# Optimization experiments

Measured on AMD Instinct MI355X. Metric: run time of the kernel, lower is better.

The kernel has to match this reference:

```python
import jax, jax.numpy as jnp
import numpy as np

B, S, N, D = 4, 8, 1024, 512
PROJ_DIM = 512
HEADS = 4
EPSILON = 0.01


def pose_encoding(p):
    # p: [B,S,N,d]; faithful to PoseEncoding.__call__
    n, d = p.shape[-2], p.shape[-1]
    sin_d = d // 2 if d % 2 == 0 else (d - 1) // 2 + 1
    cos_d = d // 2 if d % 2 == 0 else (d - 1) // 2
    idx = jnp.arange(n, dtype=p.dtype)[:, None]
    ks = jnp.arange(sin_d, dtype=p.dtype)[None, :]
    kc = jnp.arange(cos_d, dtype=p.dtype)[None, :]
    sin_ape = jnp.sin(idx / (1000.0 * (2.0 * ks / d) + 0.01))  # [N, sin_d]
    cos_ape = jnp.cos(idx / (1000.0 * (2.0 * kc / d) + 0.01))  # [N, cos_d]
    pe = jnp.zeros((n, d), dtype=p.dtype)
    pe = pe.at[:, 0::2].set(sin_ape).at[:, 1::2].set(cos_ape)
    return p + pe


def setup_inputs() -> dict:
    key = jax.random.key(0)
    ks = jax.random.split(key, 5)
    x = jax.random.normal(ks[0], (B, S, N, D), dtype=jnp.float32)
    Wqkv = jax.random.normal(ks[1], (HEADS, D, 3 * D), dtype=jnp.float32) * 0.02
    bqkv = jax.random.normal(ks[2], (HEADS, 3 * D), dtype=jnp.float32) * 0.02
    Wp = jax.random.normal(ks[3], (HEADS, D, PROJ_DIM), dtype=jnp.float32) * 0.02
    bp = jax.random.normal(ks[4], (HEADS, PROJ_DIM), dtype=jnp.float32) * 0.02
    return {"x": x, "Wqkv": Wqkv, "bqkv": bqkv, "Wp": Wp, "bp": bp}


def reference(x, Wqkv, bqkv, Wp, bp):
    b, s, n, d = x.shape
    heads = Wqkv.shape[0]
    pred_proj = None
    proj = None
    for h in range(heads):  # small fixed loop over structurally distinct heads
        qkv = jax.nn.selu(jnp.einsum('bsnd,de->bsne', x, Wqkv[h]) + bqkv[h])
        qkv = qkv.reshape(b, s, n, 3, d)
        q, k, v = qkv[..., 0, :], qkv[..., 1, :], qkv[..., 2, :]
        # non-standard ordering: scale QK^T, multiply by V, THEN softmax
        qkT = jnp.einsum('bsnd,bsmd->bsnm', q, k) / d  # [B,S,N,N]
        att = jax.nn.softmax(jnp.einsum('bsnm,bsmd->bsnd', qkT, v), axis=-1)
        proj = jax.nn.gelu(jnp.einsum('bsnd,dp->bsnp', att, Wp[h]) + bp[h],
                           approximate=False)
        if pred_proj is None:
            pred_proj = proj
        else:
            proj = proj + EPSILON * pred_proj  # pred_proj stays = head-0 proj (as in source)
    return pose_encoding(proj)
```

## Files before the change

kernel.cpp:

```cpp
#include <hip/hip_runtime.h>
#include <hip/hip_bf16.h>
#include <math.h>

typedef unsigned short u16;
typedef unsigned int   u32;
typedef __bf16  v8bf  __attribute__((ext_vector_type(8)));
typedef float   v4f   __attribute__((ext_vector_type(4)));

#define EPS_H 0.01f

typedef const __attribute__((address_space(1))) void* gas_t;
typedef __attribute__((address_space(3))) void* las_t;
#define GL2LDS(g,l) __builtin_amdgcn_global_load_lds((gas_t)(const void*)(g), (las_t)(void*)(l), 16, 0, 0)

#define VMW8()   asm volatile("s_waitcnt vmcnt(8)" ::: "memory")
#define VMW0()   asm volatile("s_waitcnt vmcnt(0)" ::: "memory")
#define BAR()    __builtin_amdgcn_s_barrier()
#define SCHED0() __builtin_amdgcn_sched_barrier(0)

__device__ __forceinline__ u16 f2bf(float f) {
    __bf16 h = (__bf16)f;
    return *reinterpret_cast<u16*>(&h);
}
__device__ __forceinline__ float bfs(u16 v) { return __uint_as_float(((u32)v) << 16); }
__device__ __forceinline__ float selu_f(float x) {
    const float sc = 1.0507009873554805f, al = 1.6732632423543772f;
    return x > 0.f ? sc * x : sc * al * (__expf(x) - 1.0f);
}
__device__ __forceinline__ float gelu_f(float x) {
    return 0.5f * x * (1.f + erff(x * 0.7071067811865476f));
}
__device__ __forceinline__ float pe_val(int n, int j) {
    float t = 1000.0f * ((float)(j & ~1) * (1.0f / 512.0f)) + 0.01f;
    float a = (float)n / t;
    return (j & 1) ? cosf(a) : sinf(a);
}

__device__ __forceinline__ v8bf lfrag(const u16* base, int row, int lane) {
    int g = (lane >> 4) ^ ((row >> 1) & 3);
    return *(const v8bf*)((const char*)base + row * 64 + g * 16);
}

__device__ __forceinline__ void stage2(const u16* g, size_t gstride, u16* lds, int wave, int lane) {
    const int l2 = lane >> 2;
    #pragma unroll
    for (int i = 0; i < 4; ++i) {
        const int ib  = wave * 4 + i;
        const int sub = ib >> 3;
        const int rl  = (ib & 7) * 16 + l2;
        const int gs  = (lane & 3) ^ ((rl >> 1) & 3);
        GL2LDS((const char*)(g + (size_t)rl * gstride + sub * 32) + gs * 16,
               (char*)lds + ib * 1024);
    }
}

#define COMPUTE_TILE(Abuf, Bbuf)                                                   \
    {                                                                              \
        const u16* A0 = &(Abuf)[0];    const u16* A1 = &(Abuf)[4096];              \
        const u16* B0 = &(Bbuf)[0];    const u16* B1 = &(Bbuf)[4096];              \
        v8bf b0[4], b1[4];                                                         \
        _Pragma("unroll")                                                          \
        for (int fc = 0; fc < 4; ++fc) {                                           \
            const int brow = wn * 64 + fc * 16 + (lane & 15);                      \
            b0[fc] = lfrag(B0, brow, lane);                                        \
            b1[fc] = lfrag(B1, brow, lane);                                        \
        }                                                                          \
        __builtin_amdgcn_s_setprio(1);                                             \
        _Pragma("unroll")                                                          \
        for (int fr = 0; fr < 4; ++fr) {                                           \
            const int arow = wm * 64 + fr * 16 + (lane & 15);                      \
            v8bf a0 = lfrag(A0, arow, lane);                                       \
            v8bf a1 = lfrag(A1, arow, lane);                                       \
            _Pragma("unroll")                                                      \
            for (int fc = 0; fc < 4; ++fc) {                                       \
                acc[fr][fc] = __builtin_amdgcn_mfma_f32_16x16x32_bf16(a0, b0[fc], acc[fr][fc], 0, 0, 0); \
                acc[fr][fc] = __builtin_amdgcn_mfma_f32_16x16x32_bf16(a1, b1[fc], acc[fr][fc], 0, 0, 0); \
            }                                                                      \
        }                                                                          \
        __builtin_amdgcn_s_setprio(0);                                             \
    }

__global__ __launch_bounds__(256)
void k_prep(const float* __restrict__ x, u16* __restrict__ xbf, float* __restrict__ pe,
            const float* __restrict__ Wqkv, u16* __restrict__ WqT,
            const float* __restrict__ Wp, u16* __restrict__ WpT)
{
    __shared__ float t[32][33];
    const int b = blockIdx.x, tid = threadIdx.x;
    if (b < 8192) {
        const size_t i = ((size_t)b * 256 + tid) * 8;
        float4 a = *(const float4*)&x[i];
        float4 c = *(const float4*)&x[i + 4];
        ushort4 o0, o1;
        o0.x = f2bf(a.x); o0.y = f2bf(a.y); o0.z = f2bf(a.z); o0.w = f2bf(a.w);
        o1.x = f2bf(c.x); o1.y = f2bf(c.y); o1.z = f2bf(c.z); o1.w = f2bf(c.w);
        *(ushort4*)&xbf[i] = o0;
        *(ushort4*)&xbf[i + 4] = o1;
        return;
    }
    if (b < 10240) {
        int idx = (b - 8192) * 256 + tid;
        pe[idx] = pe_val(idx >> 9, idx & 511);
        return;
    }
    const float* src; u16* dst; int rows, cols, bx, by;
    if (b < 11776) {
        int l = b - 10240, hh = l / 768, rem = l % 768;
        bx = rem % 48; by = rem / 48;
        src = Wqkv + (size_t)(hh ? 3 : 0) * 786432; dst = WqT + (size_t)hh * 786432;
        rows = 512; cols = 1536;
    } else {
        int l = b - 11776, hh = l / 256, rem = l % 256;
        bx = rem % 16; by = rem / 16;
        src = Wp + (size_t)(hh ? 3 : 0) * 262144; dst = WpT + (size_t)hh * 262144;
        rows = 512; cols = 512;
    }
    const int c0 = bx * 32, r0 = by * 32;
    #pragma unroll
    for (int i = 0; i < 4; ++i) {
        int idx = tid + i * 256;
        int rr = idx >> 5, cc = idx & 31;
        t[rr][cc] = src[(size_t)(r0 + rr) * cols + c0 + cc];
    }
    __syncthreads();
    #pragma unroll
    for (int i = 0; i < 4; ++i) {
        int idx = tid + i * 256;
        int rr = idx >> 5, cc = idx & 31;
        dst[(size_t)(c0 + rr) * rows + r0 + cc] = f2bf(t[cc][rr]);
    }
}

__global__ __launch_bounds__(256, 1)
void k1_qkv(const u16* __restrict__ xbf, const u16* __restrict__ WT,
            const float* __restrict__ bias, u16* __restrict__ q,
            u16* __restrict__ kT, u16* __restrict__ vT, const int swzstride)
{
    __shared__ u16 Als[2][8192];
    __shared__ u16 Bls[2][8192];
    const int tid = threadIdx.x, lane = tid & 63, wave = tid >> 6;
    const int orig = blockIdx.x + blockIdx.y * 12;
    const int swz  = (orig & 7) * swzstride + (orig >> 3);
    const int col0 = (swz % 12) * 128, row0 = (swz / 12) * 128;
    const int wm = wave >> 1, wn = wave & 1;
    const u16* Ab = xbf + (size_t)row0 * 512;
    const u16* Bb = WT + (size_t)col0 * 512;
    v4f acc[4][4] = {};

    stage2(Ab,      512, &Als[0][0], wave, lane);
    stage2(Bb,      512, &Bls[0][0], wave, lane);
    stage2(Ab + 64, 512, &Als[1][0], wave, lane);
    stage2(Bb + 64, 512, &Bls[1][0], wave, lane);
    for (int t = 0; t < 8; ++t) {
        const int c = t & 1;
        if (t < 7) VMW8(); else VMW0();
        BAR(); SCHED0();
        COMPUTE_TILE(Als[c], Bls[c]);
        BAR(); SCHED0();
        if (t + 2 < 8) {
            const int k0 = (t + 2) * 64;
            stage2(Ab + k0, 512, &Als[c][0], wave, lane);
            stage2(Bb + k0, 512, &Bls[c][0], wave, lane);
        }
    }

    const int region = col0 >> 9;
    #pragma unroll
    for (int fn = 0; fn < 4; ++fn) {
        const int c = col0 + wn * 64 + fn * 16 + (lane & 15);
        const float bc = bias[c];
        #pragma unroll
        for (int fm = 0; fm < 4; ++fm) {
            const int rb = row0 + wm * 64 + fm * 16 + ((lane >> 4) << 2);
            float v0 = selu_f(acc[fm][fn][0] + bc);
            float v1 = selu_f(acc[fm][fn][1] + bc);
            float v2 = selu_f(acc[fm][fn][2] + bc);
            float v3 = selu_f(acc[fm][fn][3] + bc);
            if (region == 0) {
                q[(size_t)(rb + 0) * 512 + c] = f2bf(v0);
                q[(size_t)(rb + 1) * 512 + c] = f2bf(v1);
                q[(size_t)(rb + 2) * 512 + c] = f2bf(v2);
                q[(size_t)(rb + 3) * 512 + c] = f2bf(v3);
            } else {
                ushort4 st; st.x = f2bf(v0); st.y = f2bf(v1); st.z = f2bf(v2); st.w = f2bf(v3);
                const int seq = rb >> 10, n = rb & 1023;
                u16* dst = (region == 1) ? kT : vT;
                const int cc = c - ((region == 1) ? 512 : 1024);
                *(ushort4*)&dst[(size_t)seq * 524288 + (size_t)cc * 1024 + n] = st;
            }
        }
    }
}

__global__ __launch_bounds__(256, 1)
void k2_ktv(const u16* __restrict__ kT, const u16* __restrict__ vT, u16* __restrict__ Mt)
{
    __shared__ u16 Als[2][8192];
    __shared__ u16 Bls[2][8192];
    const int tid = threadIdx.x, lane = tid & 63, wave = tid >> 6;
    const int d0 = blockIdx.x * 128, p0 = blockIdx.y * 128, seq = blockIdx.z;
    const u16* Ab = kT + (size_t)seq * 524288 + (size_t)d0 * 1024;
    const u16* Bb = vT + (size_t)seq * 524288 + (size_t)p0 * 1024;
    const int wm = wave >> 1, wn = wave & 1;
    v4f acc[4][4] = {};

    stage2(Ab,      1024, &Als[0][0], wave, lane);
    stage2(Bb,      1024, &Bls[0][0], wave, lane);
    stage2(Ab + 64, 1024, &Als[1][0], wave, lane);
    stage2(Bb + 64, 1024, &Bls[1][0], wave, lane);
    for (int t = 0; t < 16; ++t) {
        const int c = t & 1;
        if (t < 15) VMW8(); else VMW0();
        BAR(); SCHED0();
        COMPUTE_TILE(Als[c], Bls[c]);
        BAR(); SCHED0();
        if (t + 2 < 16) {
            const int m0 = (t + 2) * 64;
            stage2(Ab + m0, 1024, &Als[c][0], wave, lane);
            stage2(Bb + m0, 1024, &Bls[c][0], wave, lane);
        }
    }

    #pragma unroll
    for (int fn = 0; fn < 4; ++fn) {
        const int p = p0 + wn * 64 + fn * 16 + (lane & 15);
        #pragma unroll
        for (int fm = 0; fm < 4; ++fm) {
            const int d = d0 + wm * 64 + fm * 16 + ((lane >> 4) << 2);
            ushort4 st;
            st.x = f2bf(acc[fm][fn][0] * (1.f / 512.f));
            st.y = f2bf(acc[fm][fn][1] * (1.f / 512.f));
            st.z = f2bf(acc[fm][fn][2] * (1.f / 512.f));
            st.w = f2bf(acc[fm][fn][3] * (1.f / 512.f));
            *(ushort4*)&Mt[(size_t)seq * 262144 + (size_t)p * 512 + d] = st;
        }
    }
}

__global__ __launch_bounds__(256, 1)
void k3a_s(const u16* __restrict__ q, const u16* __restrict__ Mt, u16* __restrict__ S,
           const int swzstride)
{
    __shared__ u16 Als[2][8192];
    __shared__ u16 Bls[2][8192];
    const int tid = threadIdx.x, lane = tid & 63, wave = tid >> 6;
    const int orig = blockIdx.x + blockIdx.y * 4;
    const int swz  = (orig & 7) * swzstride + (orig >> 3);
    const int p0 = (swz % 4) * 128, row0 = (swz / 4) * 128;
    const int seq = row0 >> 10;
    const u16* Ab = q + (size_t)row0 * 512;
    const u16* Bb = Mt + (size_t)seq * 262144 + (size_t)p0 * 512;
    const int wm = wave >> 1, wn = wave & 1;
    v4f acc[4][4] = {};

    stage2(Ab,      512, &Als[0][0], wave, lane);
    stage2(Bb,      512, &Bls[0][0], wave, lane);
    stage2(Ab + 64, 512, &Als[1][0], wave, lane);
    stage2(Bb + 64, 512, &Bls[1][0], wave, lane);
    for (int t = 0; t < 8; ++t) {
        const int c = t & 1;
        if (t < 7) VMW8(); else VMW0();
        BAR(); SCHED0();
        COMPUTE_TILE(Als[c], Bls[c]);
        BAR(); SCHED0();
        if (t + 2 < 8) {
            const int k0 = (t + 2) * 64;
            stage2(Ab + k0, 512, &Als[c][0], wave, lane);
            stage2(Bb + k0, 512, &Bls[c][0], wave, lane);
        }
    }

    #pragma unroll
    for (int fn = 0; fn < 4; ++fn) {
        const int c = p0 + wn * 64 + fn * 16 + (lane & 15);
        #pragma unroll
        for (int fm = 0; fm < 4; ++fm) {
            const int rb = row0 + wm * 64 + fm * 16 + ((lane >> 4) << 2);
            S[(size_t)(rb + 0) * 512 + c] = f2bf(acc[fm][fn][0]);
            S[(size_t)(rb + 1) * 512 + c] = f2bf(acc[fm][fn][1]);
            S[(size_t)(rb + 2) * 512 + c] = f2bf(acc[fm][fn][2]);
            S[(size_t)(rb + 3) * 512 + c] = f2bf(acc[fm][fn][3]);
        }
    }
}

__global__ __launch_bounds__(512)
void k3b_sm(u16* __restrict__ S)
{
    const int row  = blockIdx.x * 8 + (threadIdx.x >> 6);
    const int lane = threadIdx.x & 63;
    u16* rp = S + (size_t)row * 512 + lane * 8;
    ushort4 u0 = *(const ushort4*)rp;
    ushort4 u1 = *(const ushort4*)(rp + 4);
    float f[8] = {bfs(u0.x), bfs(u0.y), bfs(u0.z), bfs(u0.w),
                  bfs(u1.x), bfs(u1.y), bfs(u1.z), bfs(u1.w)};
    float m = f[0];
    #pragma unroll
    for (int j = 1; j < 8; ++j) m = fmaxf(m, f[j]);
    #pragma unroll
    for (int off = 32; off > 0; off >>= 1) m = fmaxf(m, __shfl_xor(m, off));
    float s = 0.f;
    #pragma unroll
    for (int j = 0; j < 8; ++j) { f[j] = __expf(f[j] - m); s += f[j]; }
    #pragma unroll
    for (int off = 32; off > 0; off >>= 1) s += __shfl_xor(s, off);
    const float inv = 1.0f / s;
    ushort4 o0, o1;
    o0.x = f2bf(f[0] * inv); o0.y = f2bf(f[1] * inv);
    o0.z = f2bf(f[2] * inv); o0.w = f2bf(f[3] * inv);
    o1.x = f2bf(f[4] * inv); o1.y = f2bf(f[5] * inv);
    o1.z = f2bf(f[6] * inv); o1.w = f2bf(f[7] * inv);
    *(ushort4*)rp = o0;
    *(ushort4*)(rp + 4) = o1;
}

__global__ __launch_bounds__(256, 1)
void k3c_proj(const u16* __restrict__ att, const u16* __restrict__ WpT,
              const float* __restrict__ bp, const float* __restrict__ pe,
              float* __restrict__ out, const int mode, const int rowbase, const int swzstride)
{
    __shared__ u16 Als[2][8192];
    __shared__ u16 Bls[2][8192];
    const int tid = threadIdx.x, lane = tid & 63, wave = tid >> 6;
    const int orig = blockIdx.x + blockIdx.y * 4;
    const int swz  = (orig & 7) * swzstride + (orig >> 3);
    const int e0 = (swz % 4) * 128, row0 = (swz / 4) * 128;
    const u16* Ab = att + (size_t)row0 * 512;
    const u16* Bb = WpT + (size_t)e0 * 512;
    const int wm = wave >> 1, wn = wave & 1;
    v4f acc[4][4] = {};

    stage2(Ab,      512, &Als[0][0], wave, lane);
    stage2(Bb,      512, &Bls[0][0], wave, lane);
    stage2(Ab + 64, 512, &Als[1][0], wave, lane);
    stage2(Bb + 64, 512, &Bls[1][0], wave, lane);
    for (int t = 0; t < 8; ++t) {
        const int c = t & 1;
        if (t < 7) VMW8(); else VMW0();
        BAR(); SCHED0();
        COMPUTE_TILE(Als[c], Bls[c]);
        BAR(); SCHED0();
        if (t + 2 < 8) {
            const int k0 = (t + 2) * 64;
            stage2(Ab + k0, 512, &Als[c][0], wave, lane);
            stage2(Bb + k0, 512, &Bls[c][0], wave, lane);
        }
    }

    #pragma unroll
    for (int fn = 0; fn < 4; ++fn) {
        const int e = e0 + wn * 64 + fn * 16 + (lane & 15);
        const float be = bp[e];
        #pragma unroll
        for (int fm = 0; fm < 4; ++fm) {
            const int rb = row0 + wm * 64 + fm * 16 + ((lane >> 4) << 2);
            #pragma unroll
            for (int j = 0; j < 4; ++j) {
                const int r = rowbase + rb + j;
                const float g = gelu_f(acc[fm][fn][j] + be);
                const size_t o = (size_t)r * 512 + e;
                if (mode == 0) out[o] = g;
                else           out[o] = g + EPS_H * out[o] + pe[(r & 1023) * 512 + e];
            }
        }
    }
}

extern "C" void kernel_launch(void* const* d_in, const int* in_sizes, int n_in,
                              void* d_out, int out_size, void* d_ws, size_t ws_size,
                              hipStream_t stream)
{
    const float* x    = (const float*)d_in[0];
    const float* Wqkv = (const float*)d_in[1];
    const float* bqkv = (const float*)d_in[2];
    const float* Wp   = (const float*)d_in[3];
    const float* bp   = (const float*)d_in[4];
    float* out = (float*)d_out;
    char* ws = (char*)d_ws;

    const size_t FULL_NEEDED = 157286400;

    if (ws_size >= FULL_NEEDED) {
        u16*   xbf = (u16*)(ws);
        u16*   q   = (u16*)(ws + 33554432);
        u16*   kT  = (u16*)(ws + 67108864);
        u16*   vT  = (u16*)(ws + 100663296);
        u16*   Mt  = (u16*)(ws + 134217728);
        u16*   WqT = (u16*)(ws + 150994944);
        u16*   WpT = (u16*)(ws + 154140672);
        float* pe  = (float*)(ws + 155189248);
        u16*   S   = kT;

        k_prep<<<12288, 256, 0, stream>>>(x, xbf, pe, Wqkv, WqT, Wp, WpT);
        for (int p = 0; p < 2; ++p) {
            const int h = p ? 3 : 0;
            k1_qkv<<<dim3(12, 256), 256, 0, stream>>>(xbf, WqT + (size_t)p * 786432,
                                                      bqkv + (size_t)h * 1536, q, kT, vT, 384);
            k2_ktv<<<dim3(4, 4, 32), 256, 0, stream>>>(kT, vT, Mt);
            k3a_s<<<dim3(4, 256), 256, 0, stream>>>(q, Mt, S, 128);
            k3b_sm<<<4096, 512, 0, stream>>>(S);
            k3c_proj<<<dim3(4, 256), 256, 0, stream>>>(S, WpT + (size_t)p * 262144,
                                                       bp + (size_t)h * 512, pe, out, p, 0, 128);
        }
    } else {
        u16*   xbf = (u16*)(ws);
        u16*   q   = (u16*)(ws + 33554432);
        u16*   kT  = (u16*)(ws + 50331648);
        u16*   vT  = (u16*)(ws + 67108864);
        u16*   Mt  = (u16*)(ws + 83886080);
        u16*   WqT = (u16*)(ws + 92274688);
        u16*   WpT = (u16*)(ws + 95420416);
        float* pe  = (float*)(ws + 96468992);
        u16*   S   = kT;

        k_prep<<<12288, 256, 0, stream>>>(x, xbf, pe, Wqkv, WqT, Wp, WpT);
        for (int p = 0; p < 2; ++p) {
            const int h = p ? 3 : 0;
            for (int ck = 0; ck < 2; ++ck) {
                const u16* xc = xbf + (size_t)ck * 16384 * 512;
                k1_qkv<<<dim3(12, 128), 256, 0, stream>>>(xc, WqT + (size_t)p * 786432,
                                                          bqkv + (size_t)h * 1536, q, kT, vT, 192);
                k2_ktv<<<dim3(4, 4, 16), 256, 0, stream>>>(kT, vT, Mt);
                k3a_s<<<dim3(4, 128), 256, 0, stream>>>(q, Mt, S, 64);
                k3b_sm<<<2048, 512, 0, stream>>>(S);
                k3c_proj<<<dim3(4, 128), 256, 0, stream>>>(S, WpT + (size_t)p * 262144,
                                                           bp + (size_t)h * 512, pe, out, p,
                                                           ck * 16384, 64);
            }
        }
    }
}
```

Baseline: 401.4 us.

## Fuse softmax into score GEMM epilogue and defer normalization to projection

```diff
diff --git a/kernel.cpp b/kernel.cpp
--- a/kernel.cpp
+++ b/kernel.cpp
@@ -239,7 +239,7 @@
 
 __global__ __launch_bounds__(256, 1)
 void k3a_s(const u16* __restrict__ q, const u16* __restrict__ Mt, u16* __restrict__ S,
-           const int swzstride)
+           float* __restrict__ rowpart, const int nrows, const int swzstride)
 {
     __shared__ u16 Als[2][8192];
     __shared__ u16 Bls[2][8192];
@@ -270,53 +270,33 @@
         }
     }
 
-    #pragma unroll
-    for (int fn = 0; fn < 4; ++fn) {
-        const int c = p0 + wn * 64 + fn * 16 + (lane & 15);
+    const int pp = (p0 >> 7) * 2 + wn;
+    #pragma unroll
+    for (int fm = 0; fm < 4; ++fm) {
+        const int rb = row0 + wm * 64 + fm * 16 + ((lane >> 4) << 2);
         #pragma unroll
-        for (int fm = 0; fm < 4; ++fm) {
-            const int rb = row0 + wm * 64 + fm * 16 + ((lane >> 4) << 2);
-            S[(size_t)(rb + 0) * 512 + c] = f2bf(acc[fm][fn][0]);
-            S[(size_t)(rb + 1) * 512 + c] = f2bf(acc[fm][fn][1]);
-            S[(size_t)(rb + 2) * 512 + c] = f2bf(acc[fm][fn][2]);
-            S[(size_t)(rb + 3) * 512 + c] = f2bf(acc[fm][fn][3]);
-        }
-    }
-}
-
-__global__ __launch_bounds__(512)
-void k3b_sm(u16* __restrict__ S)
-{
-    const int row  = blockIdx.x * 8 + (threadIdx.x >> 6);
-    const int lane = threadIdx.x & 63;
-    u16* rp = S + (size_t)row * 512 + lane * 8;
-    ushort4 u0 = *(const ushort4*)rp;
-    ushort4 u1 = *(const ushort4*)(rp + 4);
-    float f[8] = {bfs(u0.x), bfs(u0.y), bfs(u0.z), bfs(u0.w),
-                  bfs(u1.x), bfs(u1.y), bfs(u1.z), bfs(u1.w)};
-    float m = f[0];
-    #pragma unroll
-    for (int j = 1; j < 8; ++j) m = fmaxf(m, f[j]);
-    #pragma unroll
-    for (int off = 32; off > 0; off >>= 1) m = fmaxf(m, __shfl_xor(m, off));
-    float s = 0.f;
-    #pragma unroll
-    for (int j = 0; j < 8; ++j) { f[j] = __expf(f[j] - m); s += f[j]; }
-    #pragma unroll
-    for (int off = 32; off > 0; off >>= 1) s += __shfl_xor(s, off);
-    const float inv = 1.0f / s;
-    ushort4 o0, o1;
-    o0.x = f2bf(f[0] * inv); o0.y = f2bf(f[1] * inv);
-    o0.z = f2bf(f[2] * inv); o0.w = f2bf(f[3] * inv);
-    o1.x = f2bf(f[4] * inv); o1.y = f2bf(f[5] * inv);
-    o1.z = f2bf(f[6] * inv); o1.w = f2bf(f[7] * inv);
-    *(ushort4*)rp = o0;
-    *(ushort4*)(rp + 4) = o1;
+        for (int j = 0; j < 4; ++j) {
+            float e[4];
+            #pragma unroll
+            for (int fn = 0; fn < 4; ++fn) {
+                e[fn] = __expf(acc[fm][fn][j]);
+                const int c = p0 + wn * 64 + fn * 16 + (lane & 15);
+                S[(size_t)(rb + j) * 512 + c] = f2bf(e[fn]);
+            }
+            float s = (e[0] + e[1]) + (e[2] + e[3]);
+            s += __shfl_xor(s, 1);
+            s += __shfl_xor(s, 2);
+            s += __shfl_xor(s, 4);
+            s += __shfl_xor(s, 8);
+            if ((lane & 15) == 0) rowpart[pp * nrows + rb + j] = s;
+        }
+    }
 }
 
 __global__ __launch_bounds__(256, 1)
 void k3c_proj(const u16* __restrict__ att, const u16* __restrict__ WpT,
               const float* __restrict__ bp, const float* __restrict__ pe,
+              const float* __restrict__ rowpart, const int nrows,
               float* __restrict__ out, const int mode, const int rowbase, const int swzstride)
 {
     __shared__ u16 Als[2][8192];
@@ -347,6 +327,19 @@
         }
     }
 
+    float inv[4][4];
+    #pragma unroll
+    for (int fm = 0; fm < 4; ++fm) {
+        const int rb = row0 + wm * 64 + fm * 16 + ((lane >> 4) << 2);
+        #pragma unroll
+        for (int j = 0; j < 4; ++j) {
+            float s = 0.f;
+            #pragma unroll
+            for (int pp = 0; pp < 8; ++pp) s += rowpart[pp * nrows + rb + j];
+            inv[fm][j] = 1.0f / s;
+        }
+    }
+
     #pragma unroll
     for (int fn = 0; fn < 4; ++fn) {
         const int e = e0 + wn * 64 + fn * 16 + (lane & 15);
@@ -357,7 +350,7 @@
             #pragma unroll
             for (int j = 0; j < 4; ++j) {
                 const int r = rowbase + rb + j;
-                const float g = gelu_f(acc[fm][fn][j] + be);
+                const float g = gelu_f(acc[fm][fn][j] * inv[fm][j] + be);
                 const size_t o = (size_t)r * 512 + e;
                 if (mode == 0) out[o] = g;
                 else           out[o] = g + EPS_H * out[o] + pe[(r & 1023) * 512 + e];
@@ -390,6 +383,7 @@
         u16*   WpT = (u16*)(ws + 154140672);
         float* pe  = (float*)(ws + 155189248);
         u16*   S   = kT;
+        float* rowpart = (float*)vT;
 
         k_prep<<<12288, 256, 0, stream>>>(x, xbf, pe, Wqkv, WqT, Wp, WpT);
         for (int p = 0; p < 2; ++p) {
@@ -397,10 +391,10 @@
             k1_qkv<<<dim3(12, 256), 256, 0, stream>>>(xbf, WqT + (size_t)p * 786432,
                                                       bqkv + (size_t)h * 1536, q, kT, vT, 384);
             k2_ktv<<<dim3(4, 4, 32), 256, 0, stream>>>(kT, vT, Mt);
-            k3a_s<<<dim3(4, 256), 256, 0, stream>>>(q, Mt, S, 128);
-            k3b_sm<<<4096, 512, 0, stream>>>(S);
+            k3a_s<<<dim3(4, 256), 256, 0, stream>>>(q, Mt, S, rowpart, 32768, 128);
             k3c_proj<<<dim3(4, 256), 256, 0, stream>>>(S, WpT + (size_t)p * 262144,
-                                                       bp + (size_t)h * 512, pe, out, p, 0, 128);
+                                                       bp + (size_t)h * 512, pe, rowpart, 32768,
+                                                       out, p, 0, 128);
         }
     } else {
         u16*   xbf = (u16*)(ws);
@@ -412,6 +406,7 @@
         u16*   WpT = (u16*)(ws + 95420416);
         float* pe  = (float*)(ws + 96468992);
         u16*   S   = kT;
+        float* rowpart = (float*)vT;
 
         k_prep<<<12288, 256, 0, stream>>>(x, xbf, pe, Wqkv, WqT, Wp, WpT);
         for (int p = 0; p < 2; ++p) {
@@ -421,11 +416,10 @@
                 k1_qkv<<<dim3(12, 128), 256, 0, stream>>>(xc, WqT + (size_t)p * 786432,
                                                           bqkv + (size_t)h * 1536, q, kT, vT, 192);
                 k2_ktv<<<dim3(4, 4, 16), 256, 0, stream>>>(kT, vT, Mt);
-                k3a_s<<<dim3(4, 128), 256, 0, stream>>>(q, Mt, S, 64);
-                k3b_sm<<<2048, 512, 0, stream>>>(S);
+                k3a_s<<<dim3(4, 128), 256, 0, stream>>>(q, Mt, S, rowpart, 16384, 64);
                 k3c_proj<<<dim3(4, 128), 256, 0, stream>>>(S, WpT + (size_t)p * 262144,
-                                                           bp + (size_t)h * 512, pe, out, p,
-                                                           ck * 16384, 64);
+                                                           bp + (size_t)h * 512, pe, rowpart, 16384,
+                                                           out, p, ck * 16384, 64);
             }
         }
     }
```

Result: no change. 399.1 us, median of 2 (-0.6%).
